# Optimization experiments

Hardware: AMD Instinct MI355X
Metric: run time of the kernel (lower is better)

Reference implementation:

```python
import jax, jax.numpy as jnp
import numpy as np

B, H, W, D = 32, 56, 56, 192
WS, NH, SHIFT = 7, 6, 3
DH = D // NH          # head dim = 32
N = WS * WS           # 49 tokens per window
NW = (H // WS) * (W // WS)  # 64 windows per image
EPS = 1e-5


def _rel_pos_index():
    coords = np.stack(np.meshgrid(np.arange(WS), np.arange(WS), indexing='ij'))  # (2,WS,WS)
    flat = coords.reshape(2, -1)
    rel = flat[:, :, None] - flat[:, None, :]            # (2,N,N)
    rel = rel.transpose(1, 2, 0).astype(np.int64)        # (N,N,2)
    rel[..., 0] += WS - 1
    rel[..., 1] += WS - 1
    rel[..., 0] *= 2 * WS - 1
    return rel.sum(-1)                                    # (N,N) in [0,169)


def _shift_mask():
    img = np.zeros((H, W))
    bounds = [(0, H - WS), (H - WS, H - SHIFT), (H - SHIFT, H)]
    cnt = 0
    for h0, h1 in bounds:
        for w0, w1 in bounds:
            img[h0:h1, w0:w1] = cnt
            cnt += 1
    win = img.reshape(H // WS, WS, W // WS, WS).transpose(0, 2, 1, 3).reshape(-1, N)  # (nW,N)
    diff = win[:, None, :] - win[:, :, None]
    return np.where(diff != 0, -100.0, 0.0).astype(np.float32)  # (nW,N,N)


_REL_IDX = jnp.asarray(_rel_pos_index())
_MASK = jnp.asarray(_shift_mask())


def _layernorm(x, g, b):
    mu = jnp.mean(x, -1, keepdims=True)
    var = jnp.mean(jnp.square(x - mu), -1, keepdims=True)
    return (x - mu) * jax.lax.rsqrt(var + EPS) * g + b


def _window_partition(x):  # (B,H,W,C) -> (B*nW, N, C)
    Bx, _, _, C = x.shape
    x = x.reshape(Bx, H // WS, WS, W // WS, WS, C).transpose(0, 1, 3, 2, 4, 5)
    return x.reshape(-1, N, C)


def _window_reverse(w):  # (B*nW, N, C) -> (B,H,W,C)
    C = w.shape[-1]
    x = w.reshape(-1, H // WS, W // WS, WS, WS, C).transpose(0, 1, 3, 2, 4, 5)
    return x.reshape(-1, H, W, C)


def setup_inputs() -> dict:
    key = jax.random.key(0)
    ks = jax.random.split(key, 8)
    s = 0.02
    return {
        'x': jax.random.normal(ks[0], (B, H * W, D), jnp.float32),
        'norm1_g': jnp.ones((D,), jnp.float32),
        'norm1_b': jnp.zeros((D,), jnp.float32),
        'qkv_w': jax.random.normal(ks[1], (D, 3 * D), jnp.float32) * s,
        'qkv_b': jnp.zeros((3 * D,), jnp.float32),
        'proj_wo': jax.random.normal(ks[2], (D, D), jnp.float32) * s,
        'proj_bo': jnp.zeros((D,), jnp.float32),
        'rpb': jax.random.normal(ks[3], ((2 * WS - 1) ** 2, NH), jnp.float32) * s,
        'pl_w': jax.random.normal(ks[4], (NH, NH), jnp.float32) * s,
        'pl_b': jnp.zeros((NH,), jnp.float32),
        'pw_w': jax.random.normal(ks[5], (NH, NH), jnp.float32) * s,
        'pw_b': jnp.zeros((NH,), jnp.float32),
        'norm2_g': jnp.ones((D,), jnp.float32),
        'norm2_b': jnp.zeros((D,), jnp.float32),
        'fc1_w': jax.random.normal(ks[6], (D, 4 * D), jnp.float32) * s,
        'fc1_b': jnp.zeros((4 * D,), jnp.float32),
        'fc2_w': jax.random.normal(ks[7], (4 * D, D), jnp.float32) * s,
        'fc2_b': jnp.zeros((D,), jnp.float32),
    }


def reference(x, norm1_g, norm1_b, qkv_w, qkv_b, proj_wo, proj_bo, rpb,
              pl_w, pl_b, pw_w, pw_b, norm2_g, norm2_b,
              fc1_w, fc1_b, fc2_w, fc2_b):
    shortcut = x
    h = _layernorm(x, norm1_g, norm1_b).reshape(B, H, W, D)
    h = jnp.roll(h, (-SHIFT, -SHIFT), (1, 2))             # shifted windows
    win = _window_partition(h)                            # (B_, N, D), B_ = B*NW
    B_ = win.shape[0]

    qkv = win @ qkv_w + qkv_b                             # (B_, N, 3D)
    q_out, k_out, v_out = qkv[..., :D], qkv[..., D:2 * D], qkv[..., 2 * D:]
    qkv5 = qkv.reshape(B_, N, 3, NH, DH)
    q = qkv5[:, :, 0].transpose(0, 2, 1, 3)               # (B_, H, N, d)
    k = qkv5[:, :, 1].transpose(0, 2, 1, 3)
    v = qkv5[:, :, 2].transpose(0, 2, 1, 3)

    scale = DH ** -0.5
    attn = jnp.einsum('bhnd,bhmd->bhnm', q * scale, k)    # (B_, H, N, N)
    bias = rpb[_REL_IDX.reshape(-1)].reshape(N, N, NH).transpose(2, 0, 1)
    attn = attn + bias[None]
    # proj_l over the head axis (distillation transform, pre-softmax)
    attn = jnp.einsum('bhnm,hg->bgnm', attn, pl_w) + pl_b[None, :, None, None]
    # shifted-window mask
    attn = attn.reshape(B, NW, NH, N, N) + _MASK[None, :, None]
    attn = jax.nn.softmax(attn.reshape(B_, NH, N, N), axis=-1)
    # proj_w over the head axis (post-softmax)
    attn = jnp.einsum('bhnm,hg->bgnm', attn, pw_w) + pw_b[None, :, None, None]

    out = jnp.einsum('bhnm,bhmd->bnhd', attn, v).reshape(B_, N, D)
    out = out @ proj_wo + proj_bo

    h = _window_reverse(out)                              # (B,H,W,D)
    h = jnp.roll(h, (SHIFT, SHIFT), (1, 2)).reshape(B, H * W, D)
    xo = shortcut + h

    m = _layernorm(xo, norm2_g, norm2_b)
    m = jax.nn.gelu(m @ fc1_w + fc1_b, approximate=False) @ fc2_w + fc2_b
    xo = xo + m
    return xo, (q_out, k_out, v_out)
```

## Files before the change

kernel.cpp:

```cpp
#include <hip/hip_runtime.h>
#include <math.h>

#define TOK   100352
#define OUTCH 19267584L
#define NWIN  2048

typedef __attribute__((ext_vector_type(4))) float f32x4;
typedef __attribute__((ext_vector_type(8))) short bf16x8;

__device__ __forceinline__ unsigned short f2bf(float f) {
    unsigned u = __builtin_bit_cast(unsigned, f);
    u += 0x7FFFu + ((u >> 16) & 1u);
    return (unsigned short)(u >> 16);
}
__device__ __forceinline__ float bf2f(unsigned short s) {
    return __builtin_bit_cast(float, (unsigned)s << 16);
}

__global__ __launch_bounds__(256) void k_prep_w(const float* __restrict__ qkv_w,
                                                const float* __restrict__ proj_w,
                                                const float* __restrict__ fc1_w,
                                                const float* __restrict__ fc2_w,
                                                unsigned short* __restrict__ wt)
{
    int i = blockIdx.x * 256 + threadIdx.x;
    float v;
    if (i < 110592) {
        int instr = i >> 9, rem = i & 511, lane = rem >> 3, j = rem & 7;
        int ks = instr % 6, t = instr / 6;
        int ni = t % 3, t2 = t / 3;
        int wv = t2 & 3, s = t2 >> 2;
        int n = s * 192 + wv * 48 + ni * 16 + (lane & 15);
        int k = ks * 32 + ((lane >> 4) << 3) + j;
        v = qkv_w[k * 576 + n];
    } else if (i < 147456) {
        int j2 = i - 110592;
        int instr = j2 >> 9, rem = j2 & 511, lane = rem >> 3, j = rem & 7;
        int ks = instr % 6, t = instr / 6;
        int ni = t % 3, wv = t / 3;
        int n = wv * 48 + ni * 16 + (lane & 15);
        int k = ks * 32 + ((lane >> 4) << 3) + j;
        v = proj_w[k * 192 + n];
    } else if (i < 294912) {
        int j2 = i - 147456;
        int instr = j2 >> 9, rem = j2 & 511, lane = rem >> 3, j = rem & 7;
        int ks = instr % 6, t = instr / 6;
        int ni = t % 3, t2 = t / 3;
        int wv = t2 & 3, s = t2 >> 2;
        int n = s * 192 + wv * 48 + ni * 16 + (lane & 15);
        int k = ks * 32 + ((lane >> 4) << 3) + j;
        v = fc1_w[k * 768 + n];
    } else {
        int j2 = i - 294912;
        int instr = j2 >> 9, rem = j2 & 511, lane = rem >> 3, j = rem & 7;
        int ks = instr % 6, t = instr / 6;
        int ni = t % 3, t2 = t / 3;
        int wv = t2 & 3, s = t2 >> 2;
        int n = wv * 48 + ni * 16 + (lane & 15);
        int k = s * 192 + ks * 32 + ((lane >> 4) << 3) + j;
        v = fc2_w[k * 192 + n];
    }
    wt[i] = f2bf(v);
}

__global__ __launch_bounds__(256) void k_qkv(const float* __restrict__ x,
                                             const float* __restrict__ g,
                                             const float* __restrict__ b,
                                             const unsigned short* __restrict__ wp,
                                             const float* __restrict__ bias,
                                             float* __restrict__ outq)
{
    __shared__ unsigned short lA[64 * 192];
    const int tid = threadIdx.x, lane = tid & 63, wv = tid >> 6;
    const int s = blockIdx.x;
    const long m0 = (long)blockIdx.y * 64;

    {
        int r = tid >> 2, c0 = (tid & 3) * 48;
        int t = (int)m0 + r;
        int w = t / 49, n = t - w * 49;
        int bb = w >> 6, widx = w & 63;
        int wi = widx >> 3, wj = widx & 7;
        int rr = n / 7, ss = n - rr * 7;
        int hh = wi * 7 + rr + 3; if (hh >= 56) hh -= 56;
        int ww = wj * 7 + ss + 3; if (ww >= 56) ww -= 56;
        const f32x4* sp = (const f32x4*)(x + ((long)(bb * 56 + hh) * 56 + ww) * 192 + c0);
        f32x4 vv[12];
        float sum = 0.f, sq = 0.f;
        #pragma unroll
        for (int i = 0; i < 12; i++) {
            vv[i] = sp[i];
            #pragma unroll
            for (int j = 0; j < 4; j++) { sum += vv[i][j]; sq += vv[i][j] * vv[i][j]; }
        }
        sum += __shfl_xor(sum, 1); sq += __shfl_xor(sq, 1);
        sum += __shfl_xor(sum, 2); sq += __shfl_xor(sq, 2);
        float mu = sum * (1.f / 192.f);
        float rs = rsqrtf(sq * (1.f / 192.f) - mu * mu + 1e-5f);
        #pragma unroll
        for (int i = 0; i < 6; i++) {
            bf16x8 o8;
            #pragma unroll
            for (int j = 0; j < 8; j++) {
                int idx = i * 8 + j, c = c0 + idx;
                o8[j] = (short)f2bf((vv[idx >> 2][idx & 3] - mu) * rs * g[c] + b[c]);
            }
            *(bf16x8*)((char*)lA + r * 384 + ((2 * (c0 + i * 8)) ^ ((r & 7) << 4))) = o8;
        }
    }
    __syncthreads();

    f32x4 acc[4][3];
    #pragma unroll
    for (int mi = 0; mi < 4; mi++)
        #pragma unroll
        for (int ni = 0; ni < 3; ni++) acc[mi][ni] = (f32x4){0.f, 0.f, 0.f, 0.f};
    #pragma unroll
    for (int ks = 0; ks < 6; ks++) {
        int kb = ks * 64 + ((lane >> 4) << 4);
        bf16x8 bfr[3];
        #pragma unroll
        for (int ni = 0; ni < 3; ni++) {
            int instr = ((s * 4 + wv) * 3 + ni) * 6 + ks;
            bfr[ni] = *(const bf16x8*)(wp + (instr << 9) + (lane << 3));
        }
        #pragma unroll
        for (int mi = 0; mi < 4; mi++) {
            int row = mi * 16 + (lane & 15);
            bf16x8 afr = *(const bf16x8*)((char*)lA + row * 384 + (kb ^ ((row & 7) << 4)));
            #pragma unroll
            for (int ni = 0; ni < 3; ni++)
                acc[mi][ni] = __builtin_amdgcn_mfma_f32_16x16x32_bf16(afr, bfr[ni], acc[mi][ni], 0, 0, 0);
        }
    }

    #pragma unroll
    for (int mi = 0; mi < 4; mi++)
        #pragma unroll
        for (int ni = 0; ni < 3; ni++) {
            int gc = wv * 48 + ni * 16 + (lane & 15);
            float bv = bias[s * 192 + gc];
            #pragma unroll
            for (int r4 = 0; r4 < 4; r4++) {
                long lr = mi * 16 + ((lane >> 4) << 2) + r4;
                outq[(long)s * OUTCH + (m0 + lr) * 192 + gc] = acc[mi][ni][r4] + bv;
            }
        }
}

__global__ __launch_bounds__(256) void k_proj(const unsigned short* __restrict__ aspat,
                                              const unsigned short* __restrict__ wp,
                                              const float* __restrict__ pbias,
                                              const float* __restrict__ x,
                                              const float* __restrict__ g2,
                                              const float* __restrict__ b2,
                                              float* __restrict__ xo,
                                              unsigned short* __restrict__ h2)
{
    __shared__ unsigned short lA[64 * 192];
    __shared__ float xoT[64][196];
    const int tid = threadIdx.x, lane = tid & 63, wv = tid >> 6;
    const long m0 = (long)blockIdx.x * 64;

    #pragma unroll
    for (int c = tid; c < 64 * 24; c += 256) {
        int row = c / 24, k16 = c - row * 24;
        bf16x8 v = *(const bf16x8*)(aspat + (m0 + row) * 192 + k16 * 8);
        *(bf16x8*)((char*)lA + row * 384 + ((k16 * 16) ^ ((row & 7) << 4))) = v;
    }
    __syncthreads();

    f32x4 acc[4][3];
    #pragma unroll
    for (int mi = 0; mi < 4; mi++)
        #pragma unroll
        for (int ni = 0; ni < 3; ni++) acc[mi][ni] = (f32x4){0.f, 0.f, 0.f, 0.f};
    #pragma unroll
    for (int ks = 0; ks < 6; ks++) {
        int kb = ks * 64 + ((lane >> 4) << 4);
        bf16x8 bfr[3];
        #pragma unroll
        for (int ni = 0; ni < 3; ni++) {
            int instr = (wv * 3 + ni) * 6 + ks;
            bfr[ni] = *(const bf16x8*)(wp + (instr << 9) + (lane << 3));
        }
        #pragma unroll
        for (int mi = 0; mi < 4; mi++) {
            int row = mi * 16 + (lane & 15);
            bf16x8 afr = *(const bf16x8*)((char*)lA + row * 384 + (kb ^ ((row & 7) << 4)));
            #pragma unroll
            for (int ni = 0; ni < 3; ni++)
                acc[mi][ni] = __builtin_amdgcn_mfma_f32_16x16x32_bf16(afr, bfr[ni], acc[mi][ni], 0, 0, 0);
        }
    }

    #pragma unroll
    for (int mi = 0; mi < 4; mi++)
        #pragma unroll
        for (int ni = 0; ni < 3; ni++) {
            int gc = wv * 48 + ni * 16 + (lane & 15);
            float bv = pbias[gc];
            #pragma unroll
            for (int r4 = 0; r4 < 4; r4++) {
                int lr = mi * 16 + ((lane >> 4) << 2) + r4;
                long grow = m0 + lr;
                float xv = x[grow * 192 + gc] + acc[mi][ni][r4] + bv;
                xoT[lr][gc] = xv;
                xo[grow * 192 + gc] = xv;
            }
        }
    __syncthreads();

    {
        int r = tid >> 2, c0 = (tid & 3) * 48;
        float vv[48];
        float sum = 0.f, sq = 0.f;
        #pragma unroll
        for (int i = 0; i < 48; i++) { vv[i] = xoT[r][c0 + i]; sum += vv[i]; sq += vv[i] * vv[i]; }
        sum += __shfl_xor(sum, 1); sq += __shfl_xor(sq, 1);
        sum += __shfl_xor(sum, 2); sq += __shfl_xor(sq, 2);
        float mu = sum * (1.f / 192.f);
        float rs = rsqrtf(sq * (1.f / 192.f) - mu * mu + 1e-5f);
        #pragma unroll
        for (int i = 0; i < 6; i++) {
            bf16x8 o8;
            #pragma unroll
            for (int j = 0; j < 8; j++) {
                int c = c0 + i * 8 + j;
                o8[j] = (short)f2bf((vv[i * 8 + j] - mu) * rs * g2[c] + b2[c]);
            }
            *(bf16x8*)(h2 + (m0 + r) * 192 + c0 + i * 8) = o8;
        }
    }
}

__global__ __launch_bounds__(256) void k_mlp(const unsigned short* __restrict__ h2,
                                             const unsigned short* __restrict__ w1p,
                                             const float* __restrict__ b1,
                                             const unsigned short* __restrict__ w2p,
                                             const float* __restrict__ b2,
                                             float* __restrict__ xo)
{
    __shared__ unsigned short lA[64 * 192];
    __shared__ unsigned short lH[64 * 192];
    const int tid = threadIdx.x, lane = tid & 63, wv = tid >> 6;
    const long m0 = (long)blockIdx.x * 64;

    #pragma unroll
    for (int c = tid; c < 64 * 24; c += 256) {
        int row = c / 24, k16 = c - row * 24;
        bf16x8 v = *(const bf16x8*)(h2 + (m0 + row) * 192 + k16 * 8);
        *(bf16x8*)((char*)lA + row * 384 + ((k16 * 16) ^ ((row & 7) << 4))) = v;
    }

    f32x4 acc2[4][3];
    #pragma unroll
    for (int mi = 0; mi < 4; mi++)
        #pragma unroll
        for (int ni = 0; ni < 3; ni++) acc2[mi][ni] = (f32x4){0.f, 0.f, 0.f, 0.f};
    __syncthreads();

    for (int s = 0; s < 4; s++) {
        f32x4 acc1[4][3];
        #pragma unroll
        for (int mi = 0; mi < 4; mi++)
            #pragma unroll
            for (int ni = 0; ni < 3; ni++) acc1[mi][ni] = (f32x4){0.f, 0.f, 0.f, 0.f};
        #pragma unroll
        for (int ks = 0; ks < 6; ks++) {
            int kb = ks * 64 + ((lane >> 4) << 4);
            bf16x8 bfr[3];
            #pragma unroll
            for (int ni = 0; ni < 3; ni++) {
                int instr = ((s * 4 + wv) * 3 + ni) * 6 + ks;
                bfr[ni] = *(const bf16x8*)(w1p + (instr << 9) + (lane << 3));
            }
            #pragma unroll
            for (int mi = 0; mi < 4; mi++) {
                int row = mi * 16 + (lane & 15);
                bf16x8 afr = *(const bf16x8*)((char*)lA + row * 384 + (kb ^ ((row & 7) << 4)));
                #pragma unroll
                for (int ni = 0; ni < 3; ni++)
                    acc1[mi][ni] = __builtin_amdgcn_mfma_f32_16x16x32_bf16(afr, bfr[ni], acc1[mi][ni], 0, 0, 0);
            }
        }
        __syncthreads();
        #pragma unroll
        for (int mi = 0; mi < 4; mi++)
            #pragma unroll
            for (int ni = 0; ni < 3; ni++) {
                int col = wv * 48 + ni * 16 + (lane & 15);
                float bv = b1[s * 192 + col];
                #pragma unroll
                for (int r = 0; r < 4; r++) {
                    int row = mi * 16 + ((lane >> 4) << 2) + r;
                    float v = acc1[mi][ni][r] + bv;
                    float ge = 0.5f * v * (1.f + erff(v * 0.70710678118654752f));
                    *(unsigned short*)((char*)lH + row * 384 + ((2 * col) ^ ((row & 7) << 4))) = f2bf(ge);
                }
            }
        __syncthreads();
        #pragma unroll
        for (int ks = 0; ks < 6; ks++) {
            int kb = ks * 64 + ((lane >> 4) << 4);
            bf16x8 bfr[3];
            #pragma unroll
            for (int ni = 0; ni < 3; ni++) {
                int instr = ((s * 4 + wv) * 3 + ni) * 6 + ks;
                bfr[ni] = *(const bf16x8*)(w2p + (instr << 9) + (lane << 3));
            }
            #pragma unroll
            for (int mi = 0; mi < 4; mi++) {
                int row = mi * 16 + (lane & 15);
                bf16x8 afr = *(const bf16x8*)((char*)lH + row * 384 + (kb ^ ((row & 7) << 4)));
                #pragma unroll
                for (int ni = 0; ni < 3; ni++)
                    acc2[mi][ni] = __builtin_amdgcn_mfma_f32_16x16x32_bf16(afr, bfr[ni], acc2[mi][ni], 0, 0, 0);
            }
        }
    }
    #pragma unroll
    for (int mi = 0; mi < 4; mi++)
        #pragma unroll
        for (int ni = 0; ni < 3; ni++) {
            int gcol = wv * 48 + ni * 16 + (lane & 15);
            float bv = b2[gcol];
            #pragma unroll
            for (int r = 0; r < 4; r++) {
                long grow = m0 + mi * 16 + ((lane >> 4) << 2) + r;
                xo[grow * 192 + gcol] += acc2[mi][ni][r] + bv;
            }
        }
}

#define ATS 67
__global__ __launch_bounds__(384) void k_attn(const float* __restrict__ qg,
                                              const float* __restrict__ kg,
                                              const float* __restrict__ vg,
                                              const float* __restrict__ rpb,
                                              const float* __restrict__ plw,
                                              const float* __restrict__ plb,
                                              const float* __restrict__ pww,
                                              const float* __restrict__ pwb,
                                              unsigned short* __restrict__ aout)
{
    __shared__ float ATT[6][49][ATS];

    int w = blockIdx.x, widx = w & 63;
    int tid = threadIdx.x, lane = tid & 63, h = tid >> 6;
    const long base = (long)w * 49 * 192;

    bf16x8 vfr[2][2];
    #pragma unroll
    for (int kst = 0; kst < 2; kst++)
        #pragma unroll
        for (int ni = 0; ni < 2; ni++) {
            int d = ni * 16 + (lane & 15);
            #pragma unroll
            for (int j = 0; j < 8; j++) {
                int n = kst * 32 + ((lane >> 4) << 3) + j; if (n > 48) n = 48;
                vfr[kst][ni][j] = (short)f2bf(vg[base + n * 192 + h * 32 + d]);
            }
        }

    for (int c = tid; c < 6 * 49 * 15; c += 384) {
        int g2 = c / (49 * 15), rem = c - g2 * (49 * 15);
        int m = rem / 15, n = 49 + (rem - m * 15);
        ATT[g2][m][n] = 0.f;
    }

    bf16x8 qfr[4], kfr[4];
    #pragma unroll
    for (int mi = 0; mi < 4; mi++) {
        int m = mi * 16 + (lane & 15); if (m > 48) m = 48;
        const float* qp = qg + base + m * 192 + h * 32 + ((lane >> 4) << 3);
        #pragma unroll
        for (int j = 0; j < 8; j++) qfr[mi][j] = (short)f2bf(qp[j]);
    }
    #pragma unroll
    for (int ni = 0; ni < 4; ni++) {
        int n = ni * 16 + (lane & 15); if (n > 48) n = 48;
        const float* kp = kg + base + n * 192 + h * 32 + ((lane >> 4) << 3);
        #pragma unroll
        for (int j = 0; j < 8; j++) kfr[ni][j] = (short)f2bf(kp[j]);
    }
    f32x4 sa[4][4];
    #pragma unroll
    for (int ni = 0; ni < 4; ni++)
        #pragma unroll
        for (int mi = 0; mi < 4; mi++)
            sa[mi][ni] = __builtin_amdgcn_mfma_f32_16x16x32_bf16(qfr[mi], kfr[ni], (f32x4){0.f, 0.f, 0.f, 0.f}, 0, 0, 0);
    const float scale = 0.17677669529663687f;
    #pragma unroll
    for (int mi = 0; mi < 4; mi++)
        #pragma unroll
        for (int ni = 0; ni < 4; ni++)
            #pragma unroll
            for (int r = 0; r < 4; r++) {
                int m = mi * 16 + ((lane >> 4) << 2) + r, n = ni * 16 + (lane & 15);
                if (m < 49 && n < 49) {
                    int rq = m / 7, cq = m - rq * 7, rk = n / 7, ck = n - rk * 7;
                    int ridx = (rq - rk + 6) * 13 + (cq - ck + 6);
                    ATT[h][m][n] = sa[mi][ni][r] * scale + rpb[ridx * 6 + h];
                }
            }
    __syncthreads();

    int wi = widx >> 3, wj = widx & 7;
    for (int p = tid; p < 2401; p += 384) {
        int m = p / 49, n = p - m * 49;
        float a[6];
        #pragma unroll
        for (int g2 = 0; g2 < 6; g2++) a[g2] = ATT[g2][m][n];
        int rq = m / 7, cq = m - rq * 7, rk = n / 7, ck = n - rk * 7;
        int ghq = wi * 7 + rq, gwq = wj * 7 + cq, ghk = wi * 7 + rk, gwk = wj * 7 + ck;
        int regq = (ghq < 49 ? 0 : (ghq < 53 ? 1 : 2)) * 3 + (gwq < 49 ? 0 : (gwq < 53 ? 1 : 2));
        int regk = (ghk < 49 ? 0 : (ghk < 53 ? 1 : 2)) * 3 + (gwk < 49 ? 0 : (gwk < 53 ? 1 : 2));
        float msk = (regq != regk) ? -100.f : 0.f;
        #pragma unroll
        for (int g2 = 0; g2 < 6; g2++) {
            float v = plb[g2] + msk;
            #pragma unroll
            for (int h2 = 0; h2 < 6; h2++) v += a[h2] * plw[h2 * 6 + g2];
            ATT[g2][m][n] = v;
        }
    }
    __syncthreads();

    if (tid < 294) {
        int g2 = tid / 49, m = tid - g2 * 49;
        float* row = &ATT[g2][m][0];
        float mx = row[0];
        #pragma unroll
        for (int j = 1; j < 49; j++) mx = fmaxf(mx, row[j]);
        float e[49]; float sm = 0.f;
        #pragma unroll
        for (int j = 0; j < 49; j++) { e[j] = __expf(row[j] - mx); sm += e[j]; }
        float inv = 1.f / sm;
        #pragma unroll
        for (int j = 0; j < 49; j++) row[j] = e[j] * inv;
    }
    __syncthreads();

    for (int p = tid; p < 2401; p += 384) {
        int m = p / 49, n = p - m * 49;
        float a[6];
        #pragma unroll
        for (int g2 = 0; g2 < 6; g2++) a[g2] = ATT[g2][m][n];
        #pragma unroll
        for (int g2 = 0; g2 < 6; g2++) {
            float v = pwb[g2];
            #pragma unroll
            for (int h2 = 0; h2 < 6; h2++) v += a[h2] * pww[h2 * 6 + g2];
            ATT[g2][m][n] = v;
        }
    }
    __syncthreads();

    f32x4 oa[4][2];
    #pragma unroll
    for (int mi = 0; mi < 4; mi++)
        #pragma unroll
        for (int ni = 0; ni < 2; ni++) oa[mi][ni] = (f32x4){0.f, 0.f, 0.f, 0.f};
    #pragma unroll
    for (int kst = 0; kst < 2; kst++) {
        #pragma unroll
        for (int mi = 0; mi < 4; mi++) {
            int m = mi * 16 + (lane & 15); if (m > 48) m = 48;
            const float* ap = &ATT[h][m][kst * 32 + ((lane >> 4) << 3)];
            bf16x8 afr;
            #pragma unroll
            for (int j = 0; j < 8; j++) afr[j] = (short)f2bf(ap[j]);
            #pragma unroll
            for (int ni = 0; ni < 2; ni++)
                oa[mi][ni] = __builtin_amdgcn_mfma_f32_16x16x32_bf16(afr, vfr[kst][ni], oa[mi][ni], 0, 0, 0);
        }
    }
    int bb = w >> 6;
    #pragma unroll
    for (int mi = 0; mi < 4; mi++)
        #pragma unroll
        for (int ni = 0; ni < 2; ni++)
            #pragma unroll
            for (int r = 0; r < 4; r++) {
                int m = mi * 16 + ((lane >> 4) << 2) + r, d = ni * 16 + (lane & 15);
                if (m < 49) {
                    int rr = m / 7, ss = m - rr * 7;
                    int ho = wi * 7 + rr + 3; if (ho >= 56) ho -= 56;
                    int wo = wj * 7 + ss + 3; if (wo >= 56) wo -= 56;
                    long tp = ((long)(bb * 56 + ho) * 56 + wo);
                    aout[tp * 192 + h * 32 + d] = f2bf(oa[mi][ni][r]);
                }
            }
}

extern "C" void kernel_launch(void* const* d_in, const int* in_sizes, int n_in,
                              void* d_out, int out_size, void* d_ws, size_t ws_size,
                              hipStream_t stream)
{
    const float* x      = (const float*)d_in[0];
    const float* n1g    = (const float*)d_in[1];
    const float* n1b    = (const float*)d_in[2];
    const float* qkv_w  = (const float*)d_in[3];
    const float* qkv_b  = (const float*)d_in[4];
    const float* proj_w = (const float*)d_in[5];
    const float* proj_b = (const float*)d_in[6];
    const float* rpb    = (const float*)d_in[7];
    const float* pl_w   = (const float*)d_in[8];
    const float* pl_b   = (const float*)d_in[9];
    const float* pw_w   = (const float*)d_in[10];
    const float* pw_b   = (const float*)d_in[11];
    const float* n2g    = (const float*)d_in[12];
    const float* n2b    = (const float*)d_in[13];
    const float* fc1_w  = (const float*)d_in[14];
    const float* fc1_b  = (const float*)d_in[15];
    const float* fc2_w  = (const float*)d_in[16];
    const float* fc2_b  = (const float*)d_in[17];

    float* out   = (float*)d_out;
    float* out_q = out + OUTCH;
    float* out_k = out + 2 * OUTCH;
    float* out_v = out + 3 * OUTCH;

    char* ws = (char*)d_ws;
    unsigned short* bufT = (unsigned short*)ws;
    unsigned short* bufW = (unsigned short*)(ws + 38535168);

    k_prep_w<<<1728, 256, 0, stream>>>(qkv_w, proj_w, fc1_w, fc2_w, bufW);
    k_qkv<<<dim3(3, 1568), 256, 0, stream>>>(x, n1g, n1b, bufW, qkv_b, out_q);
    k_attn<<<NWIN, 384, 0, stream>>>(out_q, out_k, out_v,
                                     rpb, pl_w, pl_b, pw_w, pw_b, bufT);
    k_proj<<<1568, 256, 0, stream>>>(bufT, bufW + 110592, proj_b, x, n2g, n2b,
                                     out, bufT);
    k_mlp<<<1568, 256, 0, stream>>>(bufT, bufW + 147456, fc1_b, bufW + 294912, fc2_b, out);
}
```

Baseline: 457.7 us.

## Fuse projection and MLP kernels; store attention scores as bf16 in LDS

Merges the output-projection+LayerNorm kernel with the MLP kernel. The normalized activations now stay in shared memory and the residual stays in registers, which removes the global write and re-read of h2 and the read-modify-write of xo. Separately, the attention kernel keeps its score matrix in bf16 rather than fp32 in LDS. This shrinks LDS use and lets the PV MFMA load its A-fragments directly without conversion. The costs are larger per-block LDS in the fused kernel (about 73KB), which may limit occupancy, and reduced precision in the pre-softmax head-mixing and softmax intermediates.

```diff
diff --git a/kernel.cpp b/kernel.cpp
--- a/kernel.cpp
+++ b/kernel.cpp
@@ -148,17 +148,23 @@
         }
 }
 
-__global__ __launch_bounds__(256) void k_proj(const unsigned short* __restrict__ aspat,
-                                              const unsigned short* __restrict__ wp,
-                                              const float* __restrict__ pbias,
-                                              const float* __restrict__ x,
-                                              const float* __restrict__ g2,
-                                              const float* __restrict__ b2,
-                                              float* __restrict__ xo,
-                                              unsigned short* __restrict__ h2)
+__global__ __launch_bounds__(256) void k_projmlp(const unsigned short* __restrict__ aspat,
+                                                 const unsigned short* __restrict__ wp,
+                                                 const float* __restrict__ pbias,
+                                                 const float* __restrict__ x,
+                                                 const float* __restrict__ g2,
+                                                 const float* __restrict__ b2,
+                                                 const unsigned short* __restrict__ w1p,
+                                                 const float* __restrict__ b1,
+                                                 const unsigned short* __restrict__ w2p,
+                                                 const float* __restrict__ b2m,
+                                                 float* __restrict__ xo)
 {
-    __shared__ unsigned short lA[64 * 192];
-    __shared__ float xoT[64][196];
+    __shared__ __align__(16) char SM[74752];
+    unsigned short* lA = (unsigned short*)SM;
+    float (*xoT)[196]  = (float(*)[196])(SM + 24576);
+    unsigned short* lH = (unsigned short*)(SM + 24576);
+
     const int tid = threadIdx.x, lane = tid & 63, wv = tid >> 6;
     const long m0 = (long)blockIdx.x * 64;
 
@@ -193,7 +199,6 @@
                 acc[mi][ni] = __builtin_amdgcn_mfma_f32_16x16x32_bf16(afr, bfr[ni], acc[mi][ni], 0, 0, 0);
         }
     }
-
     #pragma unroll
     for (int mi = 0; mi < 4; mi++)
         #pragma unroll
@@ -203,10 +208,9 @@
             #pragma unroll
             for (int r4 = 0; r4 < 4; r4++) {
                 int lr = mi * 16 + ((lane >> 4) << 2) + r4;
-                long grow = m0 + lr;
-                float xv = x[grow * 192 + gc] + acc[mi][ni][r4] + bv;
+                float xv = x[(m0 + lr) * 192 + gc] + acc[mi][ni][r4] + bv;
+                acc[mi][ni][r4] = xv;
                 xoT[lr][gc] = xv;
-                xo[grow * 192 + gc] = xv;
             }
         }
     __syncthreads();
@@ -221,6 +225,7 @@
         sum += __shfl_xor(sum, 2); sq += __shfl_xor(sq, 2);
         float mu = sum * (1.f / 192.f);
         float rs = rsqrtf(sq * (1.f / 192.f) - mu * mu + 1e-5f);
+        __syncthreads();
         #pragma unroll
         for (int i = 0; i < 6; i++) {
             bf16x8 o8;
@@ -229,36 +234,16 @@
                 int c = c0 + i * 8 + j;
                 o8[j] = (short)f2bf((vv[i * 8 + j] - mu) * rs * g2[c] + b2[c]);
             }
-            *(bf16x8*)(h2 + (m0 + r) * 192 + c0 + i * 8) = o8;
-        }
-    }
-}
-
-__global__ __launch_bounds__(256) void k_mlp(const unsigned short* __restrict__ h2,
-                                             const unsigned short* __restrict__ w1p,
-                                             const float* __restrict__ b1,
-                                             const unsigned short* __restrict__ w2p,
-                                             const float* __restrict__ b2,
-                                             float* __restrict__ xo)
-{
-    __shared__ unsigned short lA[64 * 192];
-    __shared__ unsigned short lH[64 * 192];
-    const int tid = threadIdx.x, lane = tid & 63, wv = tid >> 6;
-    const long m0 = (long)blockIdx.x * 64;
-
-    #pragma unroll
-    for (int c = tid; c < 64 * 24; c += 256) {
-        int row = c / 24, k16 = c - row * 24;
-        bf16x8 v = *(const bf16x8*)(h2 + (m0 + row) * 192 + k16 * 8);
-        *(bf16x8*)((char*)lA + row * 384 + ((k16 * 16) ^ ((row & 7) << 4))) = v;
-    }
+            *(bf16x8*)((char*)lA + r * 384 + ((2 * (c0 + i * 8)) ^ ((r & 7) << 4))) = o8;
+        }
+    }
+    __syncthreads();
 
     f32x4 acc2[4][3];
     #pragma unroll
     for (int mi = 0; mi < 4; mi++)
         #pragma unroll
         for (int ni = 0; ni < 3; ni++) acc2[mi][ni] = (f32x4){0.f, 0.f, 0.f, 0.f};
-    __syncthreads();
 
     for (int s = 0; s < 4; s++) {
         f32x4 acc1[4][3];
@@ -319,21 +304,22 @@
             }
         }
     }
+
     #pragma unroll
     for (int mi = 0; mi < 4; mi++)
         #pragma unroll
         for (int ni = 0; ni < 3; ni++) {
             int gcol = wv * 48 + ni * 16 + (lane & 15);
-            float bv = b2[gcol];
+            float bv = b2m[gcol];
             #pragma unroll
             for (int r = 0; r < 4; r++) {
                 long grow = m0 + mi * 16 + ((lane >> 4) << 2) + r;
-                xo[grow * 192 + gcol] += acc2[mi][ni][r] + bv;
-            }
-        }
-}
-
-#define ATS 67
+                xo[grow * 192 + gcol] = acc[mi][ni][r] + acc2[mi][ni][r] + bv;
+            }
+        }
+}
+
+#define ATS2 72
 __global__ __launch_bounds__(384) void k_attn(const float* __restrict__ qg,
                                               const float* __restrict__ kg,
                                               const float* __restrict__ vg,
@@ -344,7 +330,7 @@
                                               const float* __restrict__ pwb,
                                               unsigned short* __restrict__ aout)
 {
-    __shared__ float ATT[6][49][ATS];
+    __shared__ unsigned short ATT[6][49][ATS2];
 
     int w = blockIdx.x, widx = w & 63;
     int tid = threadIdx.x, lane = tid & 63, h = tid >> 6;
@@ -366,7 +352,7 @@
     for (int c = tid; c < 6 * 49 * 15; c += 384) {
         int g2 = c / (49 * 15), rem = c - g2 * (49 * 15);
         int m = rem / 15, n = 49 + (rem - m * 15);
-        ATT[g2][m][n] = 0.f;
+        ATT[g2][m][n] = 0;
     }
 
     bf16x8 qfr[4], kfr[4];
@@ -401,7 +387,7 @@
                 if (m < 49 && n < 49) {
                     int rq = m / 7, cq = m - rq * 7, rk = n / 7, ck = n - rk * 7;
                     int ridx = (rq - rk + 6) * 13 + (cq - ck + 6);
-                    ATT[h][m][n] = sa[mi][ni][r] * scale + rpb[ridx * 6 + h];
+                    ATT[h][m][n] = f2bf(sa[mi][ni][r] * scale + rpb[ridx * 6 + h]);
                 }
             }
     __syncthreads();
@@ -411,7 +397,7 @@
         int m = p / 49, n = p - m * 49;
         float a[6];
         #pragma unroll
-        for (int g2 = 0; g2 < 6; g2++) a[g2] = ATT[g2][m][n];
+        for (int g2 = 0; g2 < 6; g2++) a[g2] = bf2f(ATT[g2][m][n]);
         int rq = m / 7, cq = m - rq * 7, rk = n / 7, ck = n - rk * 7;
         int ghq = wi * 7 + rq, gwq = wj * 7 + cq, ghk = wi * 7 + rk, gwk = wj * 7 + ck;
         int regq = (ghq < 49 ? 0 : (ghq < 53 ? 1 : 2)) * 3 + (gwq < 49 ? 0 : (gwq < 53 ? 1 : 2));
@@ -422,23 +408,23 @@
             float v = plb[g2] + msk;
             #pragma unroll
             for (int h2 = 0; h2 < 6; h2++) v += a[h2] * plw[h2 * 6 + g2];
-            ATT[g2][m][n] = v;
+            ATT[g2][m][n] = f2bf(v);
         }
     }
     __syncthreads();
 
     if (tid < 294) {
         int g2 = tid / 49, m = tid - g2 * 49;
-        float* row = &ATT[g2][m][0];
-        float mx = row[0];
-        #pragma unroll
-        for (int j = 1; j < 49; j++) mx = fmaxf(mx, row[j]);
+        unsigned short* row = &ATT[g2][m][0];
+        float v0 = bf2f(row[0]), mx = v0;
+        #pragma unroll
+        for (int j = 1; j < 49; j++) mx = fmaxf(mx, bf2f(row[j]));
         float e[49]; float sm = 0.f;
         #pragma unroll
-        for (int j = 0; j < 49; j++) { e[j] = __expf(row[j] - mx); sm += e[j]; }
+        for (int j = 0; j < 49; j++) { e[j] = __expf(bf2f(row[j]) - mx); sm += e[j]; }
         float inv = 1.f / sm;
         #pragma unroll
-        for (int j = 0; j < 49; j++) row[j] = e[j] * inv;
+        for (int j = 0; j < 49; j++) row[j] = f2bf(e[j] * inv);
     }
     __syncthreads();
 
@@ -446,13 +432,13 @@
         int m = p / 49, n = p - m * 49;
         float a[6];
         #pragma unroll
-        for (int g2 = 0; g2 < 6; g2++) a[g2] = ATT[g2][m][n];
+        for (int g2 = 0; g2 < 6; g2++) a[g2] = bf2f(ATT[g2][m][n]);
         #pragma unroll
         for (int g2 = 0; g2 < 6; g2++) {
             float v = pwb[g2];
             #pragma unroll
             for (int h2 = 0; h2 < 6; h2++) v += a[h2] * pww[h2 * 6 + g2];
-            ATT[g2][m][n] = v;
+            ATT[g2][m][n] = f2bf(v);
         }
     }
     __syncthreads();
@@ -467,10 +453,7 @@
         #pragma unroll
         for (int mi = 0; mi < 4; mi++) {
             int m = mi * 16 + (lane & 15); if (m > 48) m = 48;
-            const float* ap = &ATT[h][m][kst * 32 + ((lane >> 4) << 3)];
-            bf16x8 afr;
-            #pragma unroll
-            for (int j = 0; j < 8; j++) afr[j] = (short)f2bf(ap[j]);
+            bf16x8 afr = *(const bf16x8*)&ATT[h][m][kst * 32 + ((lane >> 4) << 3)];
             #pragma unroll
             for (int ni = 0; ni < 2; ni++)
                 oa[mi][ni] = __builtin_amdgcn_mfma_f32_16x16x32_bf16(afr, vfr[kst][ni], oa[mi][ni], 0, 0, 0);
@@ -530,7 +513,6 @@
     k_qkv<<<dim3(3, 1568), 256, 0, stream>>>(x, n1g, n1b, bufW, qkv_b, out_q);
     k_attn<<<NWIN, 384, 0, stream>>>(out_q, out_k, out_v,
                                      rpb, pl_w, pl_b, pw_w, pw_b, bufT);
-    k_proj<<<1568, 256, 0, stream>>>(bufT, bufW + 110592, proj_b, x, n2g, n2b,
-                                     out, bufT);
-    k_mlp<<<1568, 256, 0, stream>>>(bufT, bufW + 147456, fc1_b, bufW + 294912, fc2_b, out);
-}
+    k_projmlp<<<1568, 256, 0, stream>>>(bufT, bufW + 110592, proj_b, x, n2g, n2b,
+                                        bufW + 147456, fc1_b, bufW + 294912, fc2_b, out);
+}
```

Measured after the change: 514.2 us. +12.3%, slower.
